# Kernel tuning notes

Measured on AMD Instinct MI355X. Metric: run time of the kernel, lower is better.

Reference implementation:

```python
import jax, jax.numpy as jnp
import numpy as np

N_NODES = 50000
N_EDGES = 800000
N_ATOMS = 100
HID = 128
N_LAYERS = 3
OUT_LAYERS = 2
OUT_DIM = 1
N_GRAPHS = 1024
EPS = 1e-12  # F.normalize eps


def setup_inputs() -> dict:
    key = jax.random.key(0)
    ks = jax.random.split(key, 12)
    s = 0.05
    x_ori = jax.random.randint(ks[0], (N_NODES,), 0, N_ATOMS)
    edge_index = jax.random.randint(ks[1], (2, N_EDGES), 0, N_NODES)
    edge_attr = jax.random.normal(ks[2], (N_EDGES, 1), jnp.float32)
    batch_ids = jnp.sort(jax.random.randint(ks[3], (N_NODES,), 0, N_GRAPHS))
    embd_w = jax.random.normal(ks[4], (N_ATOMS, HID), jnp.float32) * s
    gamma_w = jnp.ones((N_LAYERS, N_ATOMS, 1), jnp.float32)  # reset_parameters sets ones
    w_atom_W = jax.random.normal(ks[5], (N_LAYERS, HID, HID), jnp.float32) * s
    w_atom_b = jax.random.normal(ks[6], (N_LAYERS, HID), jnp.float32) * s
    lin_W = jax.random.normal(ks[7], (OUT_LAYERS, HID, HID), jnp.float32) * s
    lin_b = jax.random.normal(ks[8], (OUT_LAYERS, HID), jnp.float32) * s
    wp_W = jax.random.normal(ks[9], (HID, OUT_DIM), jnp.float32) * s
    wp_b = jax.random.normal(ks[10], (OUT_DIM,), jnp.float32) * s
    return dict(x_ori=x_ori, edge_index=edge_index, edge_attr=edge_attr,
                batch_ids=batch_ids, embd_w=embd_w, gamma_w=gamma_w,
                w_atom_W=w_atom_W, w_atom_b=w_atom_b, lin_W=lin_W, lin_b=lin_b,
                wp_W=wp_W, wp_b=wp_b)


def reference(x_ori, edge_index, edge_attr, batch_ids, embd_w, gamma_w,
              w_atom_W, w_atom_b, lin_W, lin_b, wp_W, wp_b):
    src, dst = edge_index[0], edge_index[1]
    x = embd_w[x_ori]  # [N, H]
    for l in range(N_LAYERS):
        h = jax.nn.relu(x @ w_atom_W[l] + w_atom_b[l])            # [N, H]
        gam = jax.nn.sigmoid(gamma_w[l])[x_ori][dst]              # [E, 1]
        ew = jnp.exp(-gam * edge_attr ** 2)                       # [E, 1]
        msg = ew * h[src]                                         # [E, H] gather+weight
        agg = jax.ops.segment_sum(msg, dst, num_segments=N_NODES) # scatter-add
        y = agg + x
        nrm = jnp.maximum(jnp.linalg.norm(y, axis=1, keepdims=True), EPS)
        x = y / nrm                                               # F.normalize(., 2, 1)
    for i in range(OUT_LAYERS):
        x = jax.nn.relu(x @ lin_W[i] + lin_b[i])
    m_x = jax.ops.segment_sum(x, batch_ids, num_segments=N_GRAPHS)  # [G, H]
    props = m_x @ wp_W + wp_b                                      # [G, 1]
    return jnp.squeeze(props, axis=1)                              # [G]
```

## Files before the change

### kernel.cpp

```cpp
#include <hip/hip_runtime.h>
#include <hip/hip_bf16.h>
#include <math.h>

typedef __hip_bfloat16 bf16;
typedef unsigned int uint;
typedef unsigned short ushort;
typedef __attribute__((ext_vector_type(8))) short short8;
typedef __attribute__((ext_vector_type(4))) float f32x4;

#define HID 128
#define NN 50000
#define NE 800000
#define NG 1024
#define NA 100
#define CAP 64

__device__ __forceinline__ uint bf16_rne_hi(float f) {
    uint u = __float_as_uint(f);
    return (u + 0x7fffu + ((u >> 16) & 1u)) & 0xffff0000u;
}
__device__ __forceinline__ uint pack_bf16x2(float lo, float hi) {
    return (bf16_rne_hi(lo) >> 16) | bf16_rne_hi(hi);
}
__device__ __forceinline__ ushort bf16_rne(float f) {
    uint u = __float_as_uint(f);
    return (ushort)((u + 0x7fffu + ((u >> 16) & 1u)) >> 16);
}
__device__ __forceinline__ float load_f(const void* p, int i, int f32) {
    return f32 ? ((const float*)p)[i]
               : __uint_as_float((uint)((const ushort*)p)[i] << 16);
}
__device__ __forceinline__ int detect_f32(const void* emb) {
    const ushort* p = (const ushort*)emb;
    int lane = threadIdx.x & 63;
    float v = __uint_as_float((uint)p[lane * 4] << 16);
    int bad0 = (!(v == v) || fabsf(v) > 1e4f || (v != 0.0f && fabsf(v) < 1e-10f));
    float w = __uint_as_float((uint)p[lane * 4 + 2] << 16);
    int bad1 = (!(w == w) || fabsf(w) > 1e4f || (w != 0.0f && fabsf(w) < 1e-10f));
    int cnt = __popcll(__ballot(bad0)) + __popcll(__ballot(bad1));
    return cnt > 16;
}

#define SCAT_BLKS  (NE / 4 / 256)
#define EMB_BLKS   ((NN * 64) / 256)
#define PACKW_BLKS (5 * 16384 / 256)
#define CVT_CNT    (300 + 384 + 256 + 128 + 1)
#define CVT_BLKS   5
#define W1_B1      SCAT_BLKS
#define W1_B2      (W1_B1 + EMB_BLKS)
#define W1_B3      (W1_B2 + PACKW_BLKS)
#define W1_B4      (W1_B3 + CVT_BLKS)
#define W1_GRID    (W1_B4 + 1)

__global__ void work1_k(const int* __restrict__ xo, const void* __restrict__ emb,
                        const void* __restrict__ gamw, const void* __restrict__ wAW,
                        const void* __restrict__ wAb, const void* __restrict__ linW,
                        const void* __restrict__ linb, const void* __restrict__ wpW,
                        const void* __restrict__ wpb,
                        const int* __restrict__ esrc, const int* __restrict__ edst,
                        const void* __restrict__ ea,
                        uint* __restrict__ xb, ushort* __restrict__ Wp,
                        float* __restrict__ f_sgam, float* __restrict__ f_wAb,
                        float* __restrict__ f_linb, float* __restrict__ f_wp,
                        float* __restrict__ f_wpb, int* __restrict__ cursor,
                        uint* __restrict__ csr, int* __restrict__ flag) {
    int f32 = detect_f32(emb);
    int b = blockIdx.x, t = threadIdx.x;
    if (b < W1_B1) {
        int e0 = (b * 256 + t) * 4;
        int4 s4 = *(const int4*)(esrc + e0);
        int4 d4 = *(const int4*)(edst + e0);
        float a0, a1, a2, a3;
        if (f32) {
            float4 f = *(const float4*)((const float*)ea + e0);
            a0 = f.x; a1 = f.y; a2 = f.z; a3 = f.w;
        } else {
            ushort4 u = *(const ushort4*)((const ushort*)ea + e0);
            a0 = __uint_as_float((uint)u.x << 16);
            a1 = __uint_as_float((uint)u.y << 16);
            a2 = __uint_as_float((uint)u.z << 16);
            a3 = __uint_as_float((uint)u.w << 16);
        }
        int p0 = atomicAdd(&cursor[d4.x], 1);
        int p1 = atomicAdd(&cursor[d4.y], 1);
        int p2 = atomicAdd(&cursor[d4.z], 1);
        int p3 = atomicAdd(&cursor[d4.w], 1);
        if (p0 < CAP) csr[d4.x * CAP + p0] = (uint)(s4.x & 0xffff) | bf16_rne_hi(a0 * a0);
        if (p1 < CAP) csr[d4.y * CAP + p1] = (uint)(s4.y & 0xffff) | bf16_rne_hi(a1 * a1);
        if (p2 < CAP) csr[d4.z * CAP + p2] = (uint)(s4.z & 0xffff) | bf16_rne_hi(a2 * a2);
        if (p3 < CAP) csr[d4.w * CAP + p3] = (uint)(s4.w & 0xffff) | bf16_rne_hi(a3 * a3);
    } else if (b < W1_B2) {
        int g = (b - W1_B1) * 256 + t;
        int node = g >> 6, c2 = g & 63;
        int base = xo[node] * HID + c2 * 2;
        xb[g] = pack_bf16x2(load_f(emb, base, f32), load_f(emb, base + 1, f32));
    } else if (b < W1_B3) {
        int t2 = (b - W1_B2) * 256 + t;
        int i   = t2 & 7;
        int n   = (t2 >> 3) & 15;
        int q   = (t2 >> 7) & 3;
        int j16 = (t2 >> 9) & 7;
        int ks  = (t2 >> 12) & 3;
        int mat = t2 >> 14;
        int k = ks * 32 + q * 8 + i;
        int j = j16 * 16 + n;
        const void* W = (mat < 3) ? wAW : linW;
        int off = ((mat < 3) ? mat : (mat - 3)) * 16384 + k * HID + j;
        Wp[t2] = bf16_rne(load_f(W, off, f32));
    } else if (b < W1_B4) {
        int idx = (b - W1_B3) * 256 + t;
        if (idx < 300) {
            float v = load_f(gamw, idx, f32);
            f_sgam[idx] = 1.0f / (1.0f + __expf(-v));
        } else if (idx < 684) {
            f_wAb[idx - 300] = load_f(wAb, idx - 300, f32);
        } else if (idx < 940) {
            f_linb[idx - 684] = load_f(linb, idx - 684, f32);
        } else if (idx < 1068) {
            f_wp[idx - 940] = load_f(wpW, idx - 940, f32);
        } else if (idx < CVT_CNT) {
            f_wpb[0] = load_f(wpb, 0, f32);
        }
    } else {
        if (t == 0) *flag = f32;
    }
}

__device__ __forceinline__ void gemm_core(const uint* __restrict__ xb,
                                          const ushort* __restrict__ Wp,
                                          const float* __restrict__ bias,
                                          int m0, int lane,
                                          f32x4 acc0[8], f32x4 acc1[8]) {
    int ln15 = lane & 15;
    int q    = lane >> 4;
    int mA = min(m0 + ln15, NN - 1);
    int mB = min(m0 + 16 + ln15, NN - 1);
    const short8* A8 = (const short8*)xb;
    const short8* B8 = (const short8*)Wp;
#pragma unroll
    for (int j16 = 0; j16 < 8; ++j16) {
        float bv = bias[j16 * 16 + ln15];
        acc0[j16] = (f32x4){bv, bv, bv, bv};
        acc1[j16] = acc0[j16];
    }
#pragma unroll
    for (int ks = 0; ks < 4; ++ks) {
        short8 a0 = A8[mA * 16 + ks * 4 + q];
        short8 a1 = A8[mB * 16 + ks * 4 + q];
#pragma unroll
        for (int j16 = 0; j16 < 8; ++j16) {
            short8 b = B8[(ks * 8 + j16) * 64 + q * 16 + ln15];
            acc0[j16] = __builtin_amdgcn_mfma_f32_16x16x32_bf16(a0, b, acc0[j16], 0, 0, 0);
            acc1[j16] = __builtin_amdgcn_mfma_f32_16x16x32_bf16(a1, b, acc1[j16], 0, 0, 0);
        }
    }
}

#define GEMM_BLKS ((NN + 127) / 128)
__global__ __launch_bounds__(256) void gemm_mfma_k(const uint* __restrict__ xb,
                                                   const ushort* __restrict__ Wp,
                                                   const float* __restrict__ bias,
                                                   uint* __restrict__ outb) {
    int lane = threadIdx.x & 63;
    int ln15 = lane & 15, q = lane >> 4;
    int m0 = blockIdx.x * 128 + (threadIdx.x >> 6) * 32;
    f32x4 acc0[8], acc1[8];
    gemm_core(xb, Wp, bias, m0, lane, acc0, acc1);
    ushort* ob = (ushort*)outb;
#pragma unroll
    for (int reg = 0; reg < 4; ++reg) {
        int n0 = m0 + q * 4 + reg;
        int n1 = n0 + 16;
#pragma unroll
        for (int j16 = 0; j16 < 8; ++j16) {
            if (n0 < NN)
                ob[(size_t)n0 * HID + j16 * 16 + ln15] = bf16_rne(fmaxf(acc0[j16][reg], 0.0f));
            if (n1 < NN)
                ob[(size_t)n1 * HID + j16 * 16 + ln15] = bf16_rne(fmaxf(acc1[j16][reg], 0.0f));
        }
    }
}

__global__ __launch_bounds__(512) void gg_k(const int* __restrict__ cursor,
                                            const uint* __restrict__ csr,
                                            const int* __restrict__ xo,
                                            const float* __restrict__ sgam,
                                            const uint* __restrict__ hb_in,
                                            uint* __restrict__ xb,
                                            const ushort* __restrict__ Wp,
                                            const float* __restrict__ bias,
                                            uint* __restrict__ hb_out) {
    __shared__ uint lds_a[2048];
    int t = threadIdx.x;
    int w = t >> 6, lane = t & 63;
    int n0 = blockIdx.x * 32;

#pragma unroll
    for (int j4 = 0; j4 < 4; ++j4) {
        int j = w * 4 + j4;
        int n = n0 + j;
        if (n < NN) {
            int deg = min(cursor[n], CAP);
            const uint* cp = csr + n * CAP;
            float g = sgam[xo[n]];
            float ax = 0.0f, ay = 0.0f;
            for (int e = 0; e < deg; e += 8) {
                uint4 c0 = *(const uint4*)(cp + e);
                uint4 c1 = *(const uint4*)(cp + e + 4);
                uint cc[8];
                cc[0] = c0.x; cc[1] = c0.y; cc[2] = c0.z; cc[3] = c0.w;
                cc[4] = c1.x; cc[5] = c1.y; cc[6] = c1.z; cc[7] = c1.w;
#pragma unroll
                for (int i = 1; i < 8; ++i) cc[i] = (e + i < deg) ? cc[i] : cc[0];
                uint v[8];
#pragma unroll
                for (int i = 0; i < 8; ++i) v[i] = hb_in[(cc[i] & 0xffffu) * 64 + lane];
                float we[8];
#pragma unroll
                for (int i = 0; i < 8; ++i) {
                    float x = __expf(-g * __uint_as_float(cc[i] & 0xffff0000u));
                    we[i] = (e + i < deg) ? x : 0.0f;
                }
#pragma unroll
                for (int i = 0; i < 8; ++i) {
                    ax = fmaf(we[i], __uint_as_float(v[i] << 16), ax);
                    ay = fmaf(we[i], __uint_as_float(v[i] & 0xffff0000u), ay);
                }
            }
            uint xv = xb[n * 64 + lane];
            float yx = ax + __uint_as_float(xv << 16);
            float yy = ay + __uint_as_float(xv & 0xffff0000u);
            float ss = yx * yx + yy * yy;
#pragma unroll
            for (int m = 32; m; m >>= 1) ss += __shfl_xor(ss, m);
            float inv = 1.0f / fmaxf(sqrtf(ss), 1e-12f);
            uint o = pack_bf16x2(yx * inv, yy * inv);
            xb[n * 64 + lane] = o;
            int rt = j >> 4, m = j & 15;
            int ks = lane >> 4, q = (lane >> 2) & 3;
            lds_a[(((rt * 4 + ks) * 64) + q * 16 + m) * 4 + (lane & 3)] = o;
        }
    }
    __syncthreads();

    int ln15 = lane & 15, q = lane >> 4;
    const short8* A8 = (const short8*)lds_a;
    const short8* B8 = (const short8*)Wp;
    f32x4 acc[2];
    {
        float bv = bias[w * 16 + ln15];
        acc[0] = (f32x4){bv, bv, bv, bv};
        acc[1] = acc[0];
    }
#pragma unroll
    for (int ks = 0; ks < 4; ++ks) {
        short8 b = B8[(ks * 8 + w) * 64 + q * 16 + ln15];
#pragma unroll
        for (int rt = 0; rt < 2; ++rt) {
            short8 a = A8[(rt * 4 + ks) * 64 + lane];
            acc[rt] = __builtin_amdgcn_mfma_f32_16x16x32_bf16(a, b, acc[rt], 0, 0, 0);
        }
    }
    ushort* ob = (ushort*)hb_out;
#pragma unroll
    for (int rt = 0; rt < 2; ++rt) {
#pragma unroll
        for (int reg = 0; reg < 4; ++reg) {
            int n = n0 + rt * 16 + q * 4 + reg;
            if (n < NN)
                ob[(size_t)n * HID + w * 16 + ln15] = bf16_rne(fmaxf(acc[rt][reg], 0.0f));
        }
    }
}

__global__ __launch_bounds__(256) void gemm5_graph_k(const uint* __restrict__ xb,
                                                     const ushort* __restrict__ Wp,
                                                     const float* __restrict__ bias,
                                                     const float* __restrict__ wp,
                                                     const int* __restrict__ batch,
                                                     float* __restrict__ grf) {
    int lane = threadIdx.x & 63;
    int ln15 = lane & 15;
    int q    = lane >> 4;
    int m0 = blockIdx.x * 128 + (threadIdx.x >> 6) * 32;
    f32x4 acc0[8], acc1[8];
    gemm_core(xb, Wp, bias, m0, lane, acc0, acc1);
    float wpv[8];
#pragma unroll
    for (int j16 = 0; j16 < 8; ++j16) wpv[j16] = wp[j16 * 16 + ln15];
#pragma unroll
    for (int half = 0; half < 2; ++half) {
#pragma unroll
        for (int reg = 0; reg < 4; ++reg) {
            float s = 0.0f;
#pragma unroll
            for (int j16 = 0; j16 < 8; ++j16) {
                float v = half ? acc1[j16][reg] : acc0[j16][reg];
                s = fmaf(fmaxf(v, 0.0f), wpv[j16], s);
            }
#pragma unroll
            for (int m = 1; m < 16; m <<= 1) s += __shfl_xor(s, m);
            int n = m0 + half * 16 + q * 4 + reg;
            if (ln15 == 0 && n < NN) atomicAdd(&grf[batch[n]], s);
        }
    }
}

__global__ void out_k(const float* __restrict__ grf, const float* __restrict__ wpb,
                      void* __restrict__ out, const int* __restrict__ flag) {
    int g = blockIdx.x * 256 + threadIdx.x;
    if (g >= NG) return;
    float r = grf[g] + wpb[0];
    if (*flag) ((float*)out)[g] = r;
    else       ((bf16*)out)[g] = __float2bfloat16(r);
}

extern "C" void kernel_launch(void* const* d_in, const int* in_sizes, int n_in,
                              void* d_out, int out_size, void* d_ws, size_t ws_size,
                              hipStream_t stream) {
    const int*  xo    = (const int*)d_in[0];
    const int*  ei    = (const int*)d_in[1];
    const int*  src   = ei;
    const int*  dst   = ei + NE;
    const void* ea    = d_in[2];
    const int*  batch = (const int*)d_in[3];
    const void* emb   = d_in[4];
    const void* gamw  = d_in[5];
    const void* wAW   = d_in[6];
    const void* wAb   = d_in[7];
    const void* linW  = d_in[8];
    const void* linb  = d_in[9];
    const void* wpW   = d_in[10];
    const void* wpb   = d_in[11];

    uint*  xb     = (uint*)d_ws;
    uint*  hA     = xb + (size_t)NN * 64;
    uint*  hB     = hA + (size_t)NN * 64;
    uint*  csr    = hB + (size_t)NN * 64;
    int*   cursor = (int*)(csr + (size_t)NN * CAP);
    float* grf    = (float*)(cursor + NN);
    float* P      = grf + NG;
    float* f_sgam = P;
    float* f_wAb  = f_sgam + 304;
    float* f_linb = f_wAb + 384;
    float* f_wp   = f_linb + 256;
    float* f_wpb  = f_wp + 128;
    int*   flag   = (int*)(f_wpb + 8);
    ushort* Wp    = (ushort*)(flag + 8);

    hipMemsetAsync(cursor, 0, (NN + NG) * sizeof(int), stream);

    work1_k<<<W1_GRID, 256, 0, stream>>>(xo, emb, gamw, wAW, wAb, linW, linb, wpW, wpb,
                                         src, dst, ea,
                                         xb, Wp, f_sgam, f_wAb, f_linb, f_wp, f_wpb,
                                         cursor, csr, flag);

    gemm_mfma_k<<<GEMM_BLKS, 256, 0, stream>>>(xb, Wp, f_wAb, hA);

    const int GG_GRID = (NN + 31) / 32;
    gg_k<<<GG_GRID, 512, 0, stream>>>(cursor, csr, xo, f_sgam,       hA, xb,
                                      Wp + 1 * 16384, f_wAb + 128, hB);
    gg_k<<<GG_GRID, 512, 0, stream>>>(cursor, csr, xo, f_sgam + 100, hB, xb,
                                      Wp + 2 * 16384, f_wAb + 256, hA);
    gg_k<<<GG_GRID, 512, 0, stream>>>(cursor, csr, xo, f_sgam + 200, hA, xb,
                                      Wp + 3 * 16384, f_linb,       hB);

    gemm5_graph_k<<<GEMM_BLKS, 256, 0, stream>>>(hB, Wp + 4 * 16384, f_linb + HID,
                                                 f_wp, batch, grf);
    out_k<<<(NG + 255) / 256, 256, 0, stream>>>(grf, f_wpb, d_out, flag);
}
```

Measured before the change: 299.7 us.

## Merge launches into two persistent kernels synchronized by global atomic counters

Fuses the preprocessing and first GEMM into one kernel, and the three graph layers, final GEMM and output write into a second, with blocks spin-waiting on global counters instead of kernel boundaries. This removes five launch gaps and their tail effects. It relies on earlier-indexed blocks being scheduled before the waiting ones, which risks deadlock or stalls if that order is not kept. Every block must also finish a whole layer before the next layer's blocks can start. The final output write moves into the last block via a completion counter.

```diff
diff --git a/kernel.cpp b/kernel.cpp
--- a/kernel.cpp
+++ b/kernel.cpp
@@ -41,32 +41,79 @@
     return cnt > 16;
 }
 
+__device__ __forceinline__ void signal_cnt(int* c) {
+    __syncthreads();
+    if (threadIdx.x == 0) { __threadfence(); atomicAdd(c, 1); }
+}
+__device__ __forceinline__ void wait_cnt(int* c, int target) {
+    if (threadIdx.x == 0) {
+        while (atomicAdd(c, 0) < target) __builtin_amdgcn_s_sleep(8);
+        __threadfence();
+    }
+    __syncthreads();
+}
+
+__device__ __forceinline__ void gemm_core(const uint* __restrict__ xb,
+                                          const ushort* __restrict__ Wp,
+                                          const float* __restrict__ bias,
+                                          int m0, int lane,
+                                          f32x4 acc0[8], f32x4 acc1[8]) {
+    int ln15 = lane & 15;
+    int q    = lane >> 4;
+    int mA = min(m0 + ln15, NN - 1);
+    int mB = min(m0 + 16 + ln15, NN - 1);
+    const short8* A8 = (const short8*)xb;
+    const short8* B8 = (const short8*)Wp;
+#pragma unroll
+    for (int j16 = 0; j16 < 8; ++j16) {
+        float bv = bias[j16 * 16 + ln15];
+        acc0[j16] = (f32x4){bv, bv, bv, bv};
+        acc1[j16] = acc0[j16];
+    }
+#pragma unroll
+    for (int ks = 0; ks < 4; ++ks) {
+        short8 a0 = A8[mA * 16 + ks * 4 + q];
+        short8 a1 = A8[mB * 16 + ks * 4 + q];
+#pragma unroll
+        for (int j16 = 0; j16 < 8; ++j16) {
+            short8 b = B8[(ks * 8 + j16) * 64 + q * 16 + ln15];
+            acc0[j16] = __builtin_amdgcn_mfma_f32_16x16x32_bf16(a0, b, acc0[j16], 0, 0, 0);
+            acc1[j16] = __builtin_amdgcn_mfma_f32_16x16x32_bf16(a1, b, acc1[j16], 0, 0, 0);
+        }
+    }
+}
+
 #define SCAT_BLKS  (NE / 4 / 256)
 #define EMB_BLKS   ((NN * 64) / 256)
 #define PACKW_BLKS (5 * 16384 / 256)
 #define CVT_CNT    (300 + 384 + 256 + 128 + 1)
 #define CVT_BLKS   5
-#define W1_B1      SCAT_BLKS
-#define W1_B2      (W1_B1 + EMB_BLKS)
-#define W1_B3      (W1_B2 + PACKW_BLKS)
-#define W1_B4      (W1_B3 + CVT_BLKS)
-#define W1_GRID    (W1_B4 + 1)
-
-__global__ void work1_k(const int* __restrict__ xo, const void* __restrict__ emb,
-                        const void* __restrict__ gamw, const void* __restrict__ wAW,
-                        const void* __restrict__ wAb, const void* __restrict__ linW,
-                        const void* __restrict__ linb, const void* __restrict__ wpW,
-                        const void* __restrict__ wpb,
-                        const int* __restrict__ esrc, const int* __restrict__ edst,
-                        const void* __restrict__ ea,
-                        uint* __restrict__ xb, ushort* __restrict__ Wp,
-                        float* __restrict__ f_sgam, float* __restrict__ f_wAb,
-                        float* __restrict__ f_linb, float* __restrict__ f_wp,
-                        float* __restrict__ f_wpb, int* __restrict__ cursor,
-                        uint* __restrict__ csr, int* __restrict__ flag) {
-    int f32 = detect_f32(emb);
+#define GEMM_BLKS  ((NN + 127) / 128)
+#define A_B1       SCAT_BLKS
+#define A_B2       (A_B1 + EMB_BLKS)
+#define A_B3       (A_B2 + PACKW_BLKS)
+#define A_B4       (A_B3 + CVT_BLKS)
+#define A_B5       (A_B4 + 1)
+#define A_GRID     (A_B5 + GEMM_BLKS)
+#define PREP_TARGET (EMB_BLKS + PACKW_BLKS + CVT_BLKS + 1)
+
+__global__ __launch_bounds__(256) void workA_k(
+        const int* __restrict__ xo, const void* __restrict__ emb,
+        const void* __restrict__ gamw, const void* __restrict__ wAW,
+        const void* __restrict__ wAb, const void* __restrict__ linW,
+        const void* __restrict__ linb, const void* __restrict__ wpW,
+        const void* __restrict__ wpb,
+        const int* __restrict__ esrc, const int* __restrict__ edst,
+        const void* __restrict__ ea,
+        uint* __restrict__ xb, ushort* __restrict__ Wp,
+        float* __restrict__ f_sgam, float* __restrict__ f_wAb,
+        float* __restrict__ f_linb, float* __restrict__ f_wp,
+        float* __restrict__ f_wpb, int* __restrict__ cursor,
+        uint* __restrict__ csr, int* __restrict__ flag,
+        int* __restrict__ cnts, uint* __restrict__ hA) {
     int b = blockIdx.x, t = threadIdx.x;
-    if (b < W1_B1) {
+    if (b < A_B1) {
+        int f32 = detect_f32(emb);
         int e0 = (b * 256 + t) * 4;
         int4 s4 = *(const int4*)(esrc + e0);
         int4 d4 = *(const int4*)(edst + e0);
@@ -89,13 +136,16 @@
         if (p1 < CAP) csr[d4.y * CAP + p1] = (uint)(s4.y & 0xffff) | bf16_rne_hi(a1 * a1);
         if (p2 < CAP) csr[d4.z * CAP + p2] = (uint)(s4.z & 0xffff) | bf16_rne_hi(a2 * a2);
         if (p3 < CAP) csr[d4.w * CAP + p3] = (uint)(s4.w & 0xffff) | bf16_rne_hi(a3 * a3);
-    } else if (b < W1_B2) {
-        int g = (b - W1_B1) * 256 + t;
+    } else if (b < A_B2) {
+        int f32 = detect_f32(emb);
+        int g = (b - A_B1) * 256 + t;
         int node = g >> 6, c2 = g & 63;
         int base = xo[node] * HID + c2 * 2;
         xb[g] = pack_bf16x2(load_f(emb, base, f32), load_f(emb, base + 1, f32));
-    } else if (b < W1_B3) {
-        int t2 = (b - W1_B2) * 256 + t;
+        signal_cnt(&cnts[0]);
+    } else if (b < A_B3) {
+        int f32 = detect_f32(emb);
+        int t2 = (b - A_B2) * 256 + t;
         int i   = t2 & 7;
         int n   = (t2 >> 3) & 15;
         int q   = (t2 >> 7) & 3;
@@ -107,8 +157,10 @@
         const void* W = (mat < 3) ? wAW : linW;
         int off = ((mat < 3) ? mat : (mat - 3)) * 16384 + k * HID + j;
         Wp[t2] = bf16_rne(load_f(W, off, f32));
-    } else if (b < W1_B4) {
-        int idx = (b - W1_B3) * 256 + t;
+        signal_cnt(&cnts[0]);
+    } else if (b < A_B4) {
+        int f32 = detect_f32(emb);
+        int idx = (b - A_B3) * 256 + t;
         if (idx < 300) {
             float v = load_f(gamw, idx, f32);
             f_sgam[idx] = 1.0f / (1.0f + __expf(-v));
@@ -121,80 +173,46 @@
         } else if (idx < CVT_CNT) {
             f_wpb[0] = load_f(wpb, 0, f32);
         }
+        signal_cnt(&cnts[0]);
+    } else if (b < A_B5) {
+        int f32 = detect_f32(emb);
+        if (t == 0) *flag = f32;
+        signal_cnt(&cnts[0]);
     } else {
-        if (t == 0) *flag = f32;
-    }
-}
-
-__device__ __forceinline__ void gemm_core(const uint* __restrict__ xb,
-                                          const ushort* __restrict__ Wp,
-                                          const float* __restrict__ bias,
-                                          int m0, int lane,
-                                          f32x4 acc0[8], f32x4 acc1[8]) {
-    int ln15 = lane & 15;
-    int q    = lane >> 4;
-    int mA = min(m0 + ln15, NN - 1);
-    int mB = min(m0 + 16 + ln15, NN - 1);
-    const short8* A8 = (const short8*)xb;
-    const short8* B8 = (const short8*)Wp;
-#pragma unroll
-    for (int j16 = 0; j16 < 8; ++j16) {
-        float bv = bias[j16 * 16 + ln15];
-        acc0[j16] = (f32x4){bv, bv, bv, bv};
-        acc1[j16] = acc0[j16];
-    }
-#pragma unroll
-    for (int ks = 0; ks < 4; ++ks) {
-        short8 a0 = A8[mA * 16 + ks * 4 + q];
-        short8 a1 = A8[mB * 16 + ks * 4 + q];
-#pragma unroll
-        for (int j16 = 0; j16 < 8; ++j16) {
-            short8 b = B8[(ks * 8 + j16) * 64 + q * 16 + ln15];
-            acc0[j16] = __builtin_amdgcn_mfma_f32_16x16x32_bf16(a0, b, acc0[j16], 0, 0, 0);
-            acc1[j16] = __builtin_amdgcn_mfma_f32_16x16x32_bf16(a1, b, acc1[j16], 0, 0, 0);
-        }
-    }
-}
-
-#define GEMM_BLKS ((NN + 127) / 128)
-__global__ __launch_bounds__(256) void gemm_mfma_k(const uint* __restrict__ xb,
-                                                   const ushort* __restrict__ Wp,
-                                                   const float* __restrict__ bias,
-                                                   uint* __restrict__ outb) {
-    int lane = threadIdx.x & 63;
-    int ln15 = lane & 15, q = lane >> 4;
-    int m0 = blockIdx.x * 128 + (threadIdx.x >> 6) * 32;
-    f32x4 acc0[8], acc1[8];
-    gemm_core(xb, Wp, bias, m0, lane, acc0, acc1);
-    ushort* ob = (ushort*)outb;
-#pragma unroll
-    for (int reg = 0; reg < 4; ++reg) {
-        int n0 = m0 + q * 4 + reg;
-        int n1 = n0 + 16;
-#pragma unroll
-        for (int j16 = 0; j16 < 8; ++j16) {
-            if (n0 < NN)
-                ob[(size_t)n0 * HID + j16 * 16 + ln15] = bf16_rne(fmaxf(acc0[j16][reg], 0.0f));
-            if (n1 < NN)
-                ob[(size_t)n1 * HID + j16 * 16 + ln15] = bf16_rne(fmaxf(acc1[j16][reg], 0.0f));
-        }
-    }
-}
-
-__global__ __launch_bounds__(512) void gg_k(const int* __restrict__ cursor,
-                                            const uint* __restrict__ csr,
-                                            const int* __restrict__ xo,
-                                            const float* __restrict__ sgam,
-                                            const uint* __restrict__ hb_in,
-                                            uint* __restrict__ xb,
-                                            const ushort* __restrict__ Wp,
-                                            const float* __restrict__ bias,
-                                            uint* __restrict__ hb_out) {
-    __shared__ uint lds_a[2048];
+        wait_cnt(&cnts[0], PREP_TARGET);
+        int lane = t & 63;
+        int ln15 = lane & 15, q = lane >> 4;
+        int m0 = (b - A_B5) * 128 + (t >> 6) * 32;
+        f32x4 acc0[8], acc1[8];
+        gemm_core(xb, Wp, f_wAb, m0, lane, acc0, acc1);
+        ushort* ob = (ushort*)hA;
+#pragma unroll
+        for (int reg = 0; reg < 4; ++reg) {
+            int n0 = m0 + q * 4 + reg;
+            int n1 = n0 + 16;
+#pragma unroll
+            for (int j16 = 0; j16 < 8; ++j16) {
+                if (n0 < NN)
+                    ob[(size_t)n0 * HID + j16 * 16 + ln15] = bf16_rne(fmaxf(acc0[j16][reg], 0.0f));
+                if (n1 < NN)
+                    ob[(size_t)n1 * HID + j16 * 16 + ln15] = bf16_rne(fmaxf(acc1[j16][reg], 0.0f));
+            }
+        }
+    }
+}
+
+__device__ __forceinline__ void gg_body(const int* __restrict__ cursor,
+                                        const uint* __restrict__ csr,
+                                        const int* __restrict__ xo,
+                                        const float* __restrict__ sgam,
+                                        const uint* __restrict__ hb_in,
+                                        uint* __restrict__ xb,
+                                        const ushort* __restrict__ Wp,
+                                        const float* __restrict__ bias,
+                                        uint* __restrict__ hb_out,
+                                        uint* lds_a, int n0) {
     int t = threadIdx.x;
     int w = t >> 6, lane = t & 63;
-    int n0 = blockIdx.x * 32;
-
 #pragma unroll
     for (int j4 = 0; j4 < 4; ++j4) {
         int j = w * 4 + j4;
@@ -242,7 +260,6 @@
         }
     }
     __syncthreads();
-
     int ln15 = lane & 15, q = lane >> 4;
     const short8* A8 = (const short8*)lds_a;
     const short8* B8 = (const short8*)Wp;
@@ -273,46 +290,77 @@
     }
 }
 
-__global__ __launch_bounds__(256) void gemm5_graph_k(const uint* __restrict__ xb,
-                                                     const ushort* __restrict__ Wp,
-                                                     const float* __restrict__ bias,
-                                                     const float* __restrict__ wp,
-                                                     const int* __restrict__ batch,
-                                                     float* __restrict__ grf) {
-    int lane = threadIdx.x & 63;
-    int ln15 = lane & 15;
-    int q    = lane >> 4;
-    int m0 = blockIdx.x * 128 + (threadIdx.x >> 6) * 32;
-    f32x4 acc0[8], acc1[8];
-    gemm_core(xb, Wp, bias, m0, lane, acc0, acc1);
-    float wpv[8];
-#pragma unroll
-    for (int j16 = 0; j16 < 8; ++j16) wpv[j16] = wp[j16 * 16 + ln15];
-#pragma unroll
-    for (int half = 0; half < 2; ++half) {
-#pragma unroll
-        for (int reg = 0; reg < 4; ++reg) {
-            float s = 0.0f;
-#pragma unroll
-            for (int j16 = 0; j16 < 8; ++j16) {
-                float v = half ? acc1[j16][reg] : acc0[j16][reg];
-                s = fmaf(fmaxf(v, 0.0f), wpv[j16], s);
+#define GG_GRID  ((NN + 31) / 32)
+#define G5_BLKS  ((NN + 255) / 256)
+#define B_GRID   (3 * GG_GRID + G5_BLKS)
+
+__global__ __launch_bounds__(512) void workB_k(
+        const int* __restrict__ cursor, const uint* __restrict__ csr,
+        const int* __restrict__ xo, const float* __restrict__ f_sgam,
+        uint* __restrict__ xb, uint* __restrict__ hA, uint* __restrict__ hB,
+        const ushort* __restrict__ Wp,
+        const float* __restrict__ f_wAb, const float* __restrict__ f_linb,
+        const float* __restrict__ f_wp, const float* __restrict__ f_wpb,
+        const int* __restrict__ batch, float* __restrict__ grf,
+        int* __restrict__ cnts, void* __restrict__ out,
+        const int* __restrict__ flag) {
+    __shared__ uint lds_a[2048];
+    int b = blockIdx.x, t = threadIdx.x;
+    if (b < 3 * GG_GRID) {
+        int layer = (b < GG_GRID) ? 0 : (b < 2 * GG_GRID ? 1 : 2);
+        int local = b - layer * GG_GRID;
+        if (layer > 0) wait_cnt(&cnts[layer], GG_GRID);
+        const uint* hin  = (layer == 1) ? hB : hA;
+        uint* hout       = (layer == 1) ? hA : hB;
+        const float* bias = (layer < 2) ? (f_wAb + 128 * (layer + 1)) : f_linb;
+        gg_body(cursor, csr, xo, f_sgam + 100 * layer, hin, xb,
+                Wp + (layer + 1) * 16384, bias, hout, lds_a, local * 32);
+        signal_cnt(&cnts[layer + 1]);
+    } else {
+        wait_cnt(&cnts[3], GG_GRID);
+        int local = b - 3 * GG_GRID;
+        int lane = t & 63;
+        int ln15 = lane & 15, q = lane >> 4;
+        int m0 = local * 256 + (t >> 6) * 32;
+        f32x4 acc0[8], acc1[8];
+        gemm_core(hB, Wp + 4 * 16384, f_linb + HID, m0, lane, acc0, acc1);
+        float wpv[8];
+#pragma unroll
+        for (int j16 = 0; j16 < 8; ++j16) wpv[j16] = f_wp[j16 * 16 + ln15];
+#pragma unroll
+        for (int half = 0; half < 2; ++half) {
+#pragma unroll
+            for (int reg = 0; reg < 4; ++reg) {
+                float s = 0.0f;
+#pragma unroll
+                for (int j16 = 0; j16 < 8; ++j16) {
+                    float v = half ? acc1[j16][reg] : acc0[j16][reg];
+                    s = fmaf(fmaxf(v, 0.0f), wpv[j16], s);
+                }
+#pragma unroll
+                for (int m = 1; m < 16; m <<= 1) s += __shfl_xor(s, m);
+                int n = m0 + half * 16 + q * 4 + reg;
+                if (ln15 == 0 && n < NN) atomicAdd(&grf[batch[n]], s);
             }
-#pragma unroll
-            for (int m = 1; m < 16; m <<= 1) s += __shfl_xor(s, m);
-            int n = m0 + half * 16 + q * 4 + reg;
-            if (ln15 == 0 && n < NN) atomicAdd(&grf[batch[n]], s);
-        }
-    }
-}
-
-__global__ void out_k(const float* __restrict__ grf, const float* __restrict__ wpb,
-                      void* __restrict__ out, const int* __restrict__ flag) {
-    int g = blockIdx.x * 256 + threadIdx.x;
-    if (g >= NG) return;
-    float r = grf[g] + wpb[0];
-    if (*flag) ((float*)out)[g] = r;
-    else       ((bf16*)out)[g] = __float2bfloat16(r);
+        }
+        __shared__ int is_last;
+        __syncthreads();
+        if (t == 0) {
+            __threadfence();
+            is_last = (atomicAdd(&cnts[4], 1) == G5_BLKS - 1);
+        }
+        __syncthreads();
+        if (is_last) {
+            __threadfence();
+            int f32 = *flag;
+            float wb = f_wpb[0];
+            for (int g = t; g < NG; g += 512) {
+                float r = atomicAdd(&grf[g], 0.0f) + wb;
+                if (f32) ((float*)out)[g] = r;
+                else     ((bf16*)out)[g] = __float2bfloat16(r);
+            }
+        }
+    }
 }
 
 extern "C" void kernel_launch(void* const* d_in, const int* in_sizes, int n_in,
@@ -339,7 +387,8 @@
     uint*  csr    = hB + (size_t)NN * 64;
     int*   cursor = (int*)(csr + (size_t)NN * CAP);
     float* grf    = (float*)(cursor + NN);
-    float* P      = grf + NG;
+    int*   cnts   = (int*)(grf + NG);
+    float* P      = (float*)(cnts + 8);
     float* f_sgam = P;
     float* f_wAb  = f_sgam + 304;
     float* f_linb = f_wAb + 384;
@@ -348,24 +397,14 @@
     int*   flag   = (int*)(f_wpb + 8);
     ushort* Wp    = (ushort*)(flag + 8);
 
-    hipMemsetAsync(cursor, 0, (NN + NG) * sizeof(int), stream);
-
-    work1_k<<<W1_GRID, 256, 0, stream>>>(xo, emb, gamw, wAW, wAb, linW, linb, wpW, wpb,
-                                         src, dst, ea,
-                                         xb, Wp, f_sgam, f_wAb, f_linb, f_wp, f_wpb,
-                                         cursor, csr, flag);
-
-    gemm_mfma_k<<<GEMM_BLKS, 256, 0, stream>>>(xb, Wp, f_wAb, hA);
-
-    const int GG_GRID = (NN + 31) / 32;
-    gg_k<<<GG_GRID, 512, 0, stream>>>(cursor, csr, xo, f_sgam,       hA, xb,
-                                      Wp + 1 * 16384, f_wAb + 128, hB);
-    gg_k<<<GG_GRID, 512, 0, stream>>>(cursor, csr, xo, f_sgam + 100, hB, xb,
-                                      Wp + 2 * 16384, f_wAb + 256, hA);
-    gg_k<<<GG_GRID, 512, 0, stream>>>(cursor, csr, xo, f_sgam + 200, hA, xb,
-                                      Wp + 3 * 16384, f_linb,       hB);
-
-    gemm5_graph_k<<<GEMM_BLKS, 256, 0, stream>>>(hB, Wp + 4 * 16384, f_linb + HID,
-                                                 f_wp, batch, grf);
-    out_k<<<(NG + 255) / 256, 256, 0, stream>>>(grf, f_wpb, d_out, flag);
-}
+    hipMemsetAsync(cursor, 0, (NN + NG + 8) * sizeof(int), stream);
+
+    workA_k<<<A_GRID, 256, 0, stream>>>(xo, emb, gamw, wAW, wAb, linW, linb, wpW, wpb,
+                                        src, dst, ea,
+                                        xb, Wp, f_sgam, f_wAb, f_linb, f_wp, f_wpb,
+                                        cursor, csr, flag, cnts, hA);
+
+    workB_k<<<B_GRID, 512, 0, stream>>>(cursor, csr, xo, f_sgam, xb, hA, hB, Wp,
+                                        f_wAb, f_linb, f_wp, f_wpb, batch, grf,
+                                        cnts, d_out, flag);
+}
```

After: 1.032 ms. 244% more time.
